# Performance work log

Hardware: AMD Instinct MI355X
Metric: run time of the kernel (lower is better)

Reference implementation:

```python
import jax, jax.numpy as jnp
import numpy as np
from math import log, sqrt

B, L, D, H, NL = 2, 2048, 512, 8, 4
HD = D // H
BOUND = 1.0 / sqrt(5.0)  # NormalizationLayer init bound


def setup_inputs() -> dict:
    key = jax.random.key(0)
    ks = jax.random.split(key, 12)
    s = 1.0 / sqrt(D)
    return {
        "base": jax.random.normal(ks[0], (B, L, D), jnp.float32),
        "qkv_w": jax.random.normal(ks[1], (NL, 3 * D, D), jnp.float32) * s,
        "qkv_b": jax.random.normal(ks[2], (NL, 3 * D), jnp.float32) * 0.01,
        "f1_w": jax.random.normal(ks[3], (NL, D, D), jnp.float32) * s,
        "f1_b": jax.random.normal(ks[4], (NL, D), jnp.float32) * 0.01,
        "f2_w": jax.random.normal(ks[5], (NL, D, D), jnp.float32) * s,
        "f2_b": jax.random.normal(ks[6], (NL, D), jnp.float32) * 0.01,
        "n1_scale": jax.random.uniform(ks[7], (NL,), jnp.float32, -BOUND, BOUND),
        "n1_bias": jax.random.uniform(ks[8], (NL,), jnp.float32, -BOUND, BOUND),
        "n2_scale": jax.random.uniform(ks[9], (NL,), jnp.float32, -BOUND, BOUND),
        "n2_bias": jax.random.uniform(ks[10], (NL,), jnp.float32, -BOUND, BOUND),
    }


def _timing_signal(seq_dim, model_dim, seq_start=1):
    # seq_len=None path of timing_signal_1d
    nt = model_dim // 2
    inc = log(10000.0) / max(nt - 1, 1)
    inv = jnp.exp(jnp.arange(nt, dtype=jnp.float32) * (-inc))  # [nt]
    pos = jnp.arange(-seq_start, seq_dim - seq_start, dtype=jnp.float32)[:, None]  # [L,1]
    st = pos * inv[None, :]  # [L, nt]
    return jnp.concatenate([jnp.sin(st), jnp.cos(st)], axis=1)[None]  # [1, L, D]


def _norm(x, scale, bias):
    # mean/std over dims (1,2), scalar affine
    m = jnp.mean(x, axis=(1, 2), keepdims=True)
    sd = jnp.sqrt(jnp.mean((x - m) ** 2, axis=(1, 2), keepdims=True))
    return (x - m) / sd * scale + bias


def reference(base, qkv_w, qkv_b, f1_w, f1_b, f2_w, f2_b,
              n1_scale, n1_bias, n2_scale, n2_bias):
    x = base + _timing_signal(L, D).astype(base.dtype)
    for i in range(NL):
        qkv = x @ qkv_w[i].T + qkv_b[i]  # [B,L,3D]
        q, k, v = jnp.split(qkv, 3, axis=2)
        q = q.reshape(B, L, H, HD)
        k = k.reshape(B, L, H, HD)
        v = v.reshape(B, L, H, HD)
        a = jnp.einsum('blhd,bmhd->bhlm', q, k) / sqrt(HD)  # [B,H,L,L]
        a = jax.nn.softmax(a, axis=-1)
        o = jnp.einsum('bhlm,bmhd->blhd', a, v).reshape(B, L, D)
        h = _norm(o @ f1_w[i].T + f1_b[i] + x, n1_scale[i], n1_bias[i])
        x = _norm(jax.nn.relu(h @ f2_w[i].T + f2_b[i]) + h, n2_scale[i], n2_bias[i])
    return x
```

## Files before the change

kernel.cpp:

```cpp
#include <hip/hip_runtime.h>
#include <hip/hip_bf16.h>

#define DEV __device__ __forceinline__

typedef __attribute__((ext_vector_type(8))) short bf16x8;
typedef __attribute__((ext_vector_type(4))) float f32x4;
typedef __attribute__((ext_vector_type(16))) float f32x16;
typedef __attribute__((ext_vector_type(4))) unsigned short u16x4;
typedef __attribute__((ext_vector_type(8))) unsigned short u16x8;


DEV unsigned short f2bf(float f) {
  union { float f; unsigned u; } v; v.f = f;
  unsigned r = v.u + 0x7FFFu + ((v.u >> 16) & 1u);
  return (unsigned short)(r >> 16);
}

DEV float bf2f(unsigned short u) {
  union { unsigned u; float f; } v; v.u = ((unsigned)u) << 16; return v.f;
}

DEV void gload_lds16(const void* g, void* lds) {
  __builtin_amdgcn_global_load_lds(
      (const __attribute__((address_space(1))) unsigned int*)g,
      (__attribute__((address_space(3))) unsigned int*)lds, 16, 0, 0);
}

DEV int swz128(int r, int cb) { return r * 128 + (cb ^ ((r & 7) << 4)); }

__global__ __launch_bounds__(256) void cvt_kernel(const float* __restrict__ s,
                                                  unsigned short* __restrict__ d, int n4) {
  int i = blockIdx.x * 256 + threadIdx.x;
  if (i >= n4) return;
  float4 v = ((const float4*)s)[i];
  u16x4 r; r[0] = f2bf(v.x); r[1] = f2bf(v.y); r[2] = f2bf(v.z); r[3] = f2bf(v.w);
  ((u16x4*)d)[i] = r;
}

__global__ __launch_bounds__(256) void init_x_kernel(const float* __restrict__ base,
                                                     float* __restrict__ xf,
                                                     unsigned short* __restrict__ xb) {
  int i = blockIdx.x * 256 + threadIdx.x;
  int d = i & 511;
  int l = (i >> 9) & 2047;
  const float NEG_INC = -(float)(9.210340371976184 / 255.0);
  int j = d & 255;
  float w = expf((float)j * NEG_INC);
  float ang = (float)(l - 1) * w;
  float ts = (d < 256) ? sinf(ang) : cosf(ang);
  float v = base[i] + ts;
  xf[i] = v;
  xb[i] = f2bf(v);
}

template<int MODE, int BM, int BN, int WR, int WC>
__global__ __launch_bounds__(WR * WC * 64) void gemm_kernel(
    const unsigned short* __restrict__ A,
    const unsigned short* __restrict__ W,
    const float* __restrict__ bias,
    const float* __restrict__ resid,
    unsigned short* __restrict__ outb,
    unsigned short* __restrict__ vtout,
    float* __restrict__ outf,
    float* __restrict__ partials,
    int N) {
  constexpr int T = WR * WC * 64;
  constexpr int WTM = BM / WR, WTN = BN / WC;
  constexpr int MR = WTM / 16, NR = WTN / 16;
  constexpr int IA = BM * 8 / T, IB = BN * 8 / T;
  __shared__ __align__(16) unsigned short Al[2][BM * 64];
  __shared__ __align__(16) unsigned short Bl[2][BN * 64];
  __shared__ float red[WR * WC * 2];
  const int tid = threadIdx.x;
  const int lane = tid & 63, wid = tid >> 6;
  const int wr = wid / WC, wc = wid % WC;
  const int m0 = blockIdx.y * BM, n0 = blockIdx.x * BN;

  auto stage = [&](int kt, int buf) {
#pragma unroll
    for (int it = 0; it < IA; ++it) {
      int c = it * T + tid;
      int row = c >> 3, sub = c & 7;
      gload_lds16((const char*)A + (m0 + row) * 1024 + kt * 128 + sub * 16,
                  (char*)Al[buf] + (it * T + wid * 64) * 16);
    }
#pragma unroll
    for (int it = 0; it < IB; ++it) {
      int c = it * T + tid;
      int row = c >> 3, sub = c & 7;
      gload_lds16((const char*)W + (n0 + row) * 1024 + kt * 128 + sub * 16,
                  (char*)Bl[buf] + (it * T + wid * 64) * 16);
    }
  };

  f32x4 acc[MR][NR];
#pragma unroll
  for (int m = 0; m < MR; ++m)
#pragma unroll
    for (int n = 0; n < NR; ++n) acc[m][n] = (f32x4){0.f, 0.f, 0.f, 0.f};

  stage(0, 0);
  __syncthreads();
  for (int kt = 0; kt < 8; ++kt) {
    int cur = kt & 1;
    if (kt < 7) stage(kt + 1, cur ^ 1);
#pragma unroll
    for (int ks = 0; ks < 2; ++ks) {
      bf16x8 af[MR], bfr[NR];
#pragma unroll
      for (int m = 0; m < MR; ++m)
        af[m] = *(const bf16x8*)&Al[cur][(wr * WTM + m * 16 + (lane & 15)) * 64 + ks * 32 + (lane >> 4) * 8];
#pragma unroll
      for (int n = 0; n < NR; ++n)
        bfr[n] = *(const bf16x8*)&Bl[cur][(wc * WTN + n * 16 + (lane & 15)) * 64 + ks * 32 + (lane >> 4) * 8];
      __builtin_amdgcn_s_setprio(1);
#pragma unroll
      for (int m = 0; m < MR; ++m)
#pragma unroll
        for (int n = 0; n < NR; ++n)
          acc[m][n] = __builtin_amdgcn_mfma_f32_16x16x32_bf16(af[m], bfr[n], acc[m][n], 0, 0, 0);
      __builtin_amdgcn_s_setprio(0);
    }
    __syncthreads();
  }

  float ps = 0.f, ps2 = 0.f;
#pragma unroll
  for (int m = 0; m < MR; ++m) {
    int row = m0 + wr * WTM + m * 16 + ((lane >> 4) << 2);
#pragma unroll
    for (int n = 0; n < NR; ++n) {
      int col = n0 + wc * WTN + n * 16 + (lane & 15);
      float bv = bias[col];
      if (MODE == 0) {
        u16x4 q4;
#pragma unroll
        for (int j = 0; j < 4; ++j) {
          float v = acc[m][n][j] + bv;
          if (col < 512) v *= 0.180336880f;
          unsigned short bf = f2bf(v);
          q4[j] = bf;
          outb[(row + j) * N + col] = bf;
        }
        if (col >= 1024) {
          int c2 = col - 1024;
          size_t va = ((size_t)((row >> 11) * 8 + (c2 >> 6)) * 64 + (c2 & 63)) * 2048 + (row & 2047);
          *(u16x4*)&vtout[va] = q4;
        }
      } else {
#pragma unroll
        for (int j = 0; j < 4; ++j) {
          float v = acc[m][n][j] + bv;
          if (MODE == 2) v = fmaxf(v, 0.f);
          int idx = (row + j) * N + col;
          v += resid[idx];
          outf[idx] = v;
          ps += v; ps2 += v * v;
        }
      }
    }
  }
  if (MODE != 0) {
#pragma unroll
    for (int s = 1; s < 64; s <<= 1) {
      ps += __shfl_xor(ps, s);
      ps2 += __shfl_xor(ps2, s);
    }
    if (lane == 0) { red[wid * 2] = ps; red[wid * 2 + 1] = ps2; }
    __syncthreads();
    if (tid == 0) {
      float s = 0.f, s2 = 0.f;
#pragma unroll
      for (int w = 0; w < WR * WC; ++w) { s += red[w * 2]; s2 += red[w * 2 + 1]; }
      constexpr int YPB = 2048 / BM;
      constexpr int SLOTS = YPB * (512 / BN);
      int batch = blockIdx.y / YPB;
      int slot = (blockIdx.y % YPB) * gridDim.x + blockIdx.x;
      partials[(batch * SLOTS + slot) * 2] = s;
      partials[(batch * SLOTS + slot) * 2 + 1] = s2;
    }
  }
}

__global__ __launch_bounds__(128) void attn_kernel(
    const unsigned short* __restrict__ qkv,
    const unsigned short* __restrict__ vT,
    unsigned short* __restrict__ op0,
    unsigned short* __restrict__ op1,
    float* __restrict__ ssums) {
  __shared__ __align__(16) unsigned short Kl[2][64 * 64];
  __shared__ __align__(16) unsigned short Vl[2][64 * 64];
  const int tid = threadIdx.x;
  const int lane = tid & 63, wid = tid >> 6;
  const int lq = lane & 31;
  const int g = lane >> 5;
  const int l0 = blockIdx.x * 64;
  const int bh = blockIdx.y;
  const int b = bh >> 3, h = bh & 7;
  const int sp = blockIdx.z;
  const int qrow = l0 + wid * 32 + lq;

  const size_t qoff = (size_t)b * 2048 * 1536 + h * 64;
  const size_t koff = qoff + 512;
  const size_t voff = (size_t)(b * 8 + h) * 64 * 2048;

  bf16x8 qf[4];
#pragma unroll
  for (int dm = 0; dm < 4; ++dm)
    qf[dm] = *(const bf16x8*)&qkv[qoff + (size_t)qrow * 1536 + dm * 16 + g * 8];

  auto stageKV = [&](int t, int buf) {
#pragma unroll
    for (int it = 0; it < 4; ++it) {
      int c = it * 128 + tid;
      int row = c >> 3, sub = c & 7;
      int sw = (sub * 16) ^ ((row & 7) << 4);
      gload_lds16((const char*)qkv + (koff + (size_t)(t * 64 + row) * 1536) * 2 + sw,
                  (char*)Kl[buf] + (it * 128 + wid * 64) * 16);
    }
#pragma unroll
    for (int it = 0; it < 4; ++it) {
      int c = it * 128 + tid;
      int row = c >> 3, sub = c & 7;
      int sw = (sub * 16) ^ ((row & 7) << 4);
      gload_lds16((const char*)vT + (voff + (size_t)row * 2048 + t * 64) * 2 + sw,
                  (char*)Vl[buf] + (it * 128 + wid * 64) * 16);
    }
  };

  stageKV(sp * 16, 0);
  __syncthreads();

  float ssum = 0.f;
  f32x16 oacc[2];
#pragma unroll
  for (int dn = 0; dn < 2; ++dn)
#pragma unroll
    for (int i = 0; i < 16; ++i) oacc[dn][i] = 0.f;

  auto pack2 = [&](const float* p, bf16x8& paA, bf16x8& paB) {
    unsigned w[8];
#pragma unroll
    for (int j = 0; j < 8; ++j)
      asm("v_cvt_pk_bf16_f32 %0, %1, %2" : "=v"(w[j]) : "v"(p[2 * j]), "v"(p[2 * j + 1]));
    asm("v_permlane32_swap_b32 %0, %1" : "+v"(w[0]), "+v"(w[2]));
    asm("v_permlane32_swap_b32 %0, %1" : "+v"(w[1]), "+v"(w[3]));
    asm("v_permlane32_swap_b32 %0, %1" : "+v"(w[4]), "+v"(w[6]));
    asm("v_permlane32_swap_b32 %0, %1" : "+v"(w[5]), "+v"(w[7]));
    union { unsigned u[4]; bf16x8 v; } a, c;
    a.u[0] = w[2]; a.u[1] = w[3]; a.u[2] = w[0]; a.u[3] = w[1];
    c.u[0] = w[6]; c.u[1] = w[7]; c.u[2] = w[4]; c.u[3] = w[5];
    paA = a.v; paB = c.v;
  };

  for (int tt = 0; tt < 16; ++tt) {
    int cur = tt & 1;
    if (tt < 15) stageKV(sp * 16 + tt + 1, cur ^ 1);

    f32x16 s0, s1;
#pragma unroll
    for (int i = 0; i < 16; ++i) { s0[i] = 0.f; s1[i] = 0.f; }
#pragma unroll
    for (int dm = 0; dm < 4; ++dm) {
      bf16x8 kf0 = *(const bf16x8*)((const char*)Kl[cur] + swz128(lq, dm * 32 + g * 16));
      bf16x8 kf1 = *(const bf16x8*)((const char*)Kl[cur] + swz128(32 + lq, dm * 32 + g * 16));
      __builtin_amdgcn_s_setprio(1);
      s0 = __builtin_amdgcn_mfma_f32_32x32x16_bf16(kf0, qf[dm], s0, 0, 0, 0);
      s1 = __builtin_amdgcn_mfma_f32_32x32x16_bf16(kf1, qf[dm], s1, 0, 0, 0);
      __builtin_amdgcn_s_setprio(0);
    }

    float p0[16], p1[16];
#pragma unroll
    for (int i = 0; i < 16; ++i) { p0[i] = exp2f(s0[i]); p1[i] = exp2f(s1[i]); }

    float a8[8];
#pragma unroll
    for (int i = 0; i < 8; ++i) a8[i] = (p0[i] + p0[i + 8]) + (p1[i] + p1[i + 8]);
#pragma unroll
    for (int i = 0; i < 4; ++i) a8[i] = a8[i] + a8[i + 4];
    float rs = (a8[0] + a8[1]) + (a8[2] + a8[3]);
    rs += __shfl_xor(rs, 32);
    ssum += rs;

    bf16x8 fr[4];
    pack2(p0, fr[0], fr[1]);
    pack2(p1, fr[2], fr[3]);

#pragma unroll
    for (int dn = 0; dn < 2; ++dn) {
      bf16x8 vf[4];
#pragma unroll
      for (int q = 0; q < 4; ++q)
        vf[q] = *(const bf16x8*)((const char*)Vl[cur] +
                                 swz128(dn * 32 + lq, q * 32 + (g ^ 1) * 16));
      __builtin_amdgcn_s_setprio(1);
#pragma unroll
      for (int q = 0; q < 4; ++q)
        oacc[dn] = __builtin_amdgcn_mfma_f32_32x32x16_bf16(vf[q], fr[q], oacc[dn], 0, 0, 0);
      __builtin_amdgcn_s_setprio(0);
    }
    __syncthreads();
  }

  unsigned short* op = sp ? op1 : op0;
  size_t obase = (size_t)bh * 131072;
#pragma unroll
  for (int dn = 0; dn < 2; ++dn)
#pragma unroll
    for (int ro = 0; ro < 4; ++ro) {
      int d0 = dn * 32 + ro * 8 + g * 4;
      u16x4 o4;
#pragma unroll
      for (int e = 0; e < 4; ++e) o4[e] = f2bf(oacc[dn][ro * 4 + e]);
      *(u16x4*)&op[obase + (size_t)qrow * 64 + d0] = o4;
    }
  if (lane < 32)
    ssums[(size_t)sp * 32768 + (size_t)bh * 2048 + qrow] = ssum;
}

__global__ __launch_bounds__(256) void attn_combine_kernel(
    const unsigned short* __restrict__ op0,
    const unsigned short* __restrict__ op1,
    const float* __restrict__ ssums,
    unsigned short* __restrict__ o) {
  const int tid = threadIdx.x;
  int row = blockIdx.x * 16 + (tid >> 4);
  int c0 = (tid & 15) * 4;
  float inv = 1.f / (ssums[row] + ssums[32768 + row]);
  u16x4 a0 = *(const u16x4*)&op0[(size_t)row * 64 + c0];
  u16x4 a1 = *(const u16x4*)&op1[(size_t)row * 64 + c0];
  int bh = row >> 11, l = row & 2047;
  int b = bh >> 3, h = bh & 7;
  u16x4 r;
#pragma unroll
  for (int e = 0; e < 4; ++e)
    r[e] = f2bf((bf2f(a0[e]) + bf2f(a1[e])) * inv);
  *(u16x4*)&o[((size_t)(b * 2048 + l)) * 512 + h * 64 + c0] = r;
}

__global__ __launch_bounds__(256) void norm_kernel(
    const float* __restrict__ in,
    const float* __restrict__ partials,
    int nslots,
    const float* __restrict__ scale_arr,
    const float* __restrict__ bias_arr,
    int layer,
    float* __restrict__ outf,
    unsigned short* __restrict__ outb,
    float* __restrict__ outf2) {
  int i4 = blockIdx.x * 256 + threadIdx.x;
  size_t i = (size_t)i4 * 4;
  int batch = (int)(i >> 20);
  const float* p = partials + batch * nslots * 2;
  int lane = threadIdx.x & 63;
  float s = 0.f, s2 = 0.f;
  for (int k = lane; k < nslots; k += 64) { s += p[k * 2]; s2 += p[k * 2 + 1]; }
#pragma unroll
  for (int m = 1; m < 64; m <<= 1) { s += __shfl_xor(s, m); s2 += __shfl_xor(s2, m); }
  const float invn = 1.f / 1048576.f;
  float mean = s * invn;
  float var = s2 * invn - mean * mean;
  float a = scale_arr[layer] / sqrtf(var);
  float bi = bias_arr[layer] - mean * a;
  float4 v = *(const float4*)(in + i);
  float4 r;
  r.x = v.x * a + bi; r.y = v.y * a + bi; r.z = v.z * a + bi; r.w = v.w * a + bi;
  *(float4*)(outf + i) = r;
  u16x4 rb; rb[0] = f2bf(r.x); rb[1] = f2bf(r.y); rb[2] = f2bf(r.z); rb[3] = f2bf(r.w);
  *(u16x4*)(outb + i) = rb;
  if (outf2) *(float4*)(outf2 + i) = r;
}

extern "C" void kernel_launch(void* const* d_in, const int* in_sizes, int n_in,
                              void* d_out, int out_size, void* d_ws, size_t ws_size,
                              hipStream_t stream) {
  (void)in_sizes; (void)n_in; (void)out_size; (void)ws_size;
  const float* base  = (const float*)d_in[0];
  const float* qkv_w = (const float*)d_in[1];
  const float* qkv_b = (const float*)d_in[2];
  const float* f1_w  = (const float*)d_in[3];
  const float* f1_b  = (const float*)d_in[4];
  const float* f2_w  = (const float*)d_in[5];
  const float* f2_b  = (const float*)d_in[6];
  const float* n1s   = (const float*)d_in[7];
  const float* n1b   = (const float*)d_in[8];
  const float* n2s   = (const float*)d_in[9];
  const float* n2b   = (const float*)d_in[10];

  char* ws = (char*)d_ws;
  float*          x_f32  = (float*)(ws + 0);
  unsigned short* x_bf   = (unsigned short*)(ws + (8u << 20));
  unsigned short* qkv_bf = (unsigned short*)(ws + (12u << 20));
  unsigned short* o_bf   = (unsigned short*)(ws + (12u << 20));
  unsigned short* h_bf   = (unsigned short*)(ws + (16u << 20));
  unsigned short* vT     = (unsigned short*)(ws + (28u << 20));
  float*          ssums  = (float*)(ws + (32u << 20));
  float*          t_f32  = (float*)(ws + (28u << 20));
  float*          h_f32  = (float*)(ws + (36u << 20));
  unsigned short* op0    = (unsigned short*)(ws + (36u << 20));
  unsigned short* op1    = (unsigned short*)(ws + (40u << 20));
  unsigned short* wq     = (unsigned short*)(ws + (44u << 20));
  unsigned short* w1     = (unsigned short*)(ws + (50u << 20));
  unsigned short* w2     = (unsigned short*)(ws + (52u << 20));
  float*          parts  = (float*)(ws + (54u << 20));

  cvt_kernel<<<3072, 256, 0, stream>>>(qkv_w, wq, 786432);
  cvt_kernel<<<1024, 256, 0, stream>>>(f1_w, w1, 262144);
  cvt_kernel<<<1024, 256, 0, stream>>>(f2_w, w2, 262144);
  init_x_kernel<<<8192, 256, 0, stream>>>(base, x_f32, x_bf);

  for (int L = 0; L < 4; ++L) {
    gemm_kernel<0, 64, 128, 1, 4><<<dim3(12, 64), 256, 0, stream>>>(
        x_bf, wq + L * 786432, qkv_b + L * 1536, nullptr, qkv_bf, vT, nullptr, nullptr, 1536);
    attn_kernel<<<dim3(32, 16, 2), 128, 0, stream>>>(qkv_bf, vT, op0, op1, ssums);
    attn_combine_kernel<<<2048, 256, 0, stream>>>(op0, op1, ssums, o_bf);
    gemm_kernel<1, 32, 64, 1, 2><<<dim3(8, 128), 128, 0, stream>>>(
        o_bf, w1 + L * 262144, f1_b + L * 512, x_f32, nullptr, nullptr, t_f32, parts, 512);
    norm_kernel<<<2048, 256, 0, stream>>>(t_f32, parts, 512, n1s, n1b, L, h_f32, h_bf, nullptr);
    gemm_kernel<2, 32, 64, 1, 2><<<dim3(8, 128), 128, 0, stream>>>(
        h_bf, w2 + L * 262144, f2_b + L * 512, h_f32, nullptr, nullptr, t_f32, parts, 512);
    norm_kernel<<<2048, 256, 0, stream>>>(t_f32, parts, 512, n2s, n2b, L, x_f32, x_bf,
                                          (L == 3) ? (float*)d_out : nullptr);
  }
}
```

Baseline: 390.9 us.

## Triple-buffer GEMM and attention loads, enlarge attention blocks, MFMA row sums

Both the GEMM and the attention main loops move from double to triple LDS buffering. Each iteration now uses an explicit vmcnt wait plus a single s_barrier, replacing the two __syncthreads per iteration, so the next tile's loads overlap compute with less synchronisation. The attention kernel now uses 256 threads covering 128 query rows per block, halving the grid and sharing each K/V tile across more waves. It also computes the softmax row sums with an MFMA against a ones vector instead of VALU adds and a shuffle, and uses the raw exp2 builtin. The cost is more LDS per block, which may reduce occupancy, and a hardcoded vmcnt that depends on the per-stage load count.

Result: faster. 357.5 us (-8.5%).

```diff
diff --git a/kernel.cpp b/kernel.cpp
--- a/kernel.cpp
+++ b/kernel.cpp
@@ -68,8 +68,9 @@
   constexpr int WTM = BM / WR, WTN = BN / WC;
   constexpr int MR = WTM / 16, NR = WTN / 16;
   constexpr int IA = BM * 8 / T, IB = BN * 8 / T;
-  __shared__ __align__(16) unsigned short Al[2][BM * 64];
-  __shared__ __align__(16) unsigned short Bl[2][BN * 64];
+  static_assert(IA + IB == 6, "vmcnt immediate assumes 6 loads per stage");
+  __shared__ __align__(16) unsigned short Al[3][BM * 64];
+  __shared__ __align__(16) unsigned short Bl[3][BN * 64];
   __shared__ float red[WR * WC * 2];
   const int tid = threadIdx.x;
   const int lane = tid & 63, wid = tid >> 6;
@@ -100,10 +101,16 @@
     for (int n = 0; n < NR; ++n) acc[m][n] = (f32x4){0.f, 0.f, 0.f, 0.f};
 
   stage(0, 0);
-  __syncthreads();
   for (int kt = 0; kt < 8; ++kt) {
-    int cur = kt & 1;
-    if (kt < 7) stage(kt + 1, cur ^ 1);
+    int cur = kt % 3;
+    if (kt < 7) {
+      stage(kt + 1, (kt + 1) % 3);
+      asm volatile("s_waitcnt vmcnt(6)" ::: "memory");
+    } else {
+      asm volatile("s_waitcnt vmcnt(0)" ::: "memory");
+    }
+    __builtin_amdgcn_s_barrier();
+    asm volatile("" ::: "memory");
 #pragma unroll
     for (int ks = 0; ks < 2; ++ks) {
       bf16x8 af[MR], bfr[NR];
@@ -121,7 +128,6 @@
           acc[m][n] = __builtin_amdgcn_mfma_f32_16x16x32_bf16(af[m], bfr[n], acc[m][n], 0, 0, 0);
       __builtin_amdgcn_s_setprio(0);
     }
-    __syncthreads();
   }
 
   float ps = 0.f, ps2 = 0.f;
@@ -182,19 +188,19 @@
   }
 }
 
-__global__ __launch_bounds__(128) void attn_kernel(
+__global__ __launch_bounds__(256) void attn_kernel(
     const unsigned short* __restrict__ qkv,
     const unsigned short* __restrict__ vT,
     unsigned short* __restrict__ op0,
     unsigned short* __restrict__ op1,
     float* __restrict__ ssums) {
-  __shared__ __align__(16) unsigned short Kl[2][64 * 64];
-  __shared__ __align__(16) unsigned short Vl[2][64 * 64];
+  __shared__ __align__(16) unsigned short Kl[3][64 * 64];
+  __shared__ __align__(16) unsigned short Vl[3][64 * 64];
   const int tid = threadIdx.x;
   const int lane = tid & 63, wid = tid >> 6;
   const int lq = lane & 31;
   const int g = lane >> 5;
-  const int l0 = blockIdx.x * 64;
+  const int l0 = blockIdx.x * 128;
   const int bh = blockIdx.y;
   const int b = bh >> 3, h = bh & 7;
   const int sp = blockIdx.z;
@@ -211,32 +217,31 @@
 
   auto stageKV = [&](int t, int buf) {
 #pragma unroll
-    for (int it = 0; it < 4; ++it) {
-      int c = it * 128 + tid;
+    for (int it = 0; it < 2; ++it) {
+      int c = it * 256 + tid;
       int row = c >> 3, sub = c & 7;
       int sw = (sub * 16) ^ ((row & 7) << 4);
       gload_lds16((const char*)qkv + (koff + (size_t)(t * 64 + row) * 1536) * 2 + sw,
-                  (char*)Kl[buf] + (it * 128 + wid * 64) * 16);
-    }
-#pragma unroll
-    for (int it = 0; it < 4; ++it) {
-      int c = it * 128 + tid;
+                  (char*)Kl[buf] + (it * 256 + wid * 64) * 16);
+    }
+#pragma unroll
+    for (int it = 0; it < 2; ++it) {
+      int c = it * 256 + tid;
       int row = c >> 3, sub = c & 7;
       int sw = (sub * 16) ^ ((row & 7) << 4);
       gload_lds16((const char*)vT + (voff + (size_t)row * 2048 + t * 64) * 2 + sw,
-                  (char*)Vl[buf] + (it * 128 + wid * 64) * 16);
+                  (char*)Vl[buf] + (it * 256 + wid * 64) * 16);
     }
   };
 
-  stageKV(sp * 16, 0);
-  __syncthreads();
-
-  float ssum = 0.f;
-  f32x16 oacc[2];
-#pragma unroll
-  for (int dn = 0; dn < 2; ++dn)
-#pragma unroll
-    for (int i = 0; i < 16; ++i) oacc[dn][i] = 0.f;
+  union { unsigned short su[8]; bf16x8 v; } ou;
+#pragma unroll
+  for (int j = 0; j < 8; ++j) ou.su[j] = 0x3F80;
+  const bf16x8 onesf = ou.v;
+
+  f32x16 oacc[2], sacc;
+#pragma unroll
+  for (int i = 0; i < 16; ++i) { oacc[0][i] = 0.f; oacc[1][i] = 0.f; sacc[i] = 0.f; }
 
   auto pack2 = [&](const float* p, bf16x8& paA, bf16x8& paB) {
     unsigned w[8];
@@ -253,9 +258,17 @@
     paA = a.v; paB = c.v;
   };
 
+  stageKV(sp * 16, 0);
   for (int tt = 0; tt < 16; ++tt) {
-    int cur = tt & 1;
-    if (tt < 15) stageKV(sp * 16 + tt + 1, cur ^ 1);
+    int cur = tt % 3;
+    if (tt < 15) {
+      stageKV(sp * 16 + tt + 1, (tt + 1) % 3);
+      asm volatile("s_waitcnt vmcnt(4)" ::: "memory");
+    } else {
+      asm volatile("s_waitcnt vmcnt(0)" ::: "memory");
+    }
+    __builtin_amdgcn_s_barrier();
+    asm volatile("" ::: "memory");
 
     f32x16 s0, s1;
 #pragma unroll
@@ -272,20 +285,20 @@
 
     float p0[16], p1[16];
 #pragma unroll
-    for (int i = 0; i < 16; ++i) { p0[i] = exp2f(s0[i]); p1[i] = exp2f(s1[i]); }
-
-    float a8[8];
-#pragma unroll
-    for (int i = 0; i < 8; ++i) a8[i] = (p0[i] + p0[i + 8]) + (p1[i] + p1[i + 8]);
-#pragma unroll
-    for (int i = 0; i < 4; ++i) a8[i] = a8[i] + a8[i + 4];
-    float rs = (a8[0] + a8[1]) + (a8[2] + a8[3]);
-    rs += __shfl_xor(rs, 32);
-    ssum += rs;
+    for (int i = 0; i < 16; ++i) {
+      p0[i] = __builtin_amdgcn_exp2f(s0[i]);
+      p1[i] = __builtin_amdgcn_exp2f(s1[i]);
+    }
 
     bf16x8 fr[4];
     pack2(p0, fr[0], fr[1]);
     pack2(p1, fr[2], fr[3]);
+
+    __builtin_amdgcn_s_setprio(1);
+#pragma unroll
+    for (int q = 0; q < 4; ++q)
+      sacc = __builtin_amdgcn_mfma_f32_32x32x16_bf16(onesf, fr[q], sacc, 0, 0, 0);
+    __builtin_amdgcn_s_setprio(0);
 
 #pragma unroll
     for (int dn = 0; dn < 2; ++dn) {
@@ -300,7 +313,6 @@
         oacc[dn] = __builtin_amdgcn_mfma_f32_32x32x16_bf16(vf[q], fr[q], oacc[dn], 0, 0, 0);
       __builtin_amdgcn_s_setprio(0);
     }
-    __syncthreads();
   }
 
   unsigned short* op = sp ? op1 : op0;
@@ -316,7 +328,7 @@
       *(u16x4*)&op[obase + (size_t)qrow * 64 + d0] = o4;
     }
   if (lane < 32)
-    ssums[(size_t)sp * 32768 + (size_t)bh * 2048 + qrow] = ssum;
+    ssums[(size_t)sp * 32768 + (size_t)bh * 2048 + qrow] = sacc[0];
 }
 
 __global__ __launch_bounds__(256) void attn_combine_kernel(
@@ -413,7 +425,7 @@
   for (int L = 0; L < 4; ++L) {
     gemm_kernel<0, 64, 128, 1, 4><<<dim3(12, 64), 256, 0, stream>>>(
         x_bf, wq + L * 786432, qkv_b + L * 1536, nullptr, qkv_bf, vT, nullptr, nullptr, 1536);
-    attn_kernel<<<dim3(32, 16, 2), 128, 0, stream>>>(qkv_bf, vT, op0, op1, ssums);
+    attn_kernel<<<dim3(16, 16, 2), 256, 0, stream>>>(qkv_bf, vT, op0, op1, ssums);
     attn_combine_kernel<<<2048, 256, 0, stream>>>(op0, op1, ssums, o_bf);
     gemm_kernel<1, 32, 64, 1, 2><<<dim3(8, 128), 128, 0, stream>>>(
         o_bf, w1 + L * 262144, f1_b + L * 512, x_f32, nullptr, nullptr, t_f32, parts, 512);
```
